# Kernel optimization log

Measured on AMD Instinct MI355X. Metric: run time of the kernel, lower is better.

## Reference

```python
import jax, jax.numpy as jnp
import numpy as np

RES = 7          # pooler_resolution
SR = 2           # sampling_ratio
SCALES = (0.25, 0.125, 0.0625)  # 1/stride for the 3 FPN levels


def _bilinear(feat, ys, xs):
    # feat [C,H,W]; ys, xs [N,S,S] sample coords; returns [C,N,S,S]
    C, H, W = feat.shape
    valid = (ys > -1.0) & (ys < H) & (xs > -1.0) & (xs < W)
    y = jnp.clip(ys, 0.0, H - 1)
    x = jnp.clip(xs, 0.0, W - 1)
    y0 = jnp.floor(y).astype(jnp.int32)
    x0 = jnp.floor(x).astype(jnp.int32)
    y1 = jnp.minimum(y0 + 1, H - 1)
    x1 = jnp.minimum(x0 + 1, W - 1)
    ly = y - y0; lx = x - x0
    hy = 1.0 - ly; hx = 1.0 - lx
    v = (feat[:, y0, x0] * (hy * hx) + feat[:, y0, x1] * (hy * lx)
         + feat[:, y1, x0] * (ly * hx) + feat[:, y1, x1] * (ly * lx))
    return v * valid


def _roi_align(feat, boxes, scale):
    # feat [C,H,W], boxes [N,4] (t,l,b,r) in image coords, aligned=True
    t, l, b, r = (boxes[:, 0], boxes[:, 1], boxes[:, 2], boxes[:, 3])
    sy = t * scale - 0.5
    sx = l * scale - 0.5
    bh = (b - t) * scale / RES
    bw = (r - l) * scale / RES
    S = RES * SR
    g = (jnp.arange(S, dtype=feat.dtype) + 0.5) / SR  # sample offsets in bin units
    ys = sy[:, None] + g[None, :] * bh[:, None]  # [N,S]
    xs = sx[:, None] + g[None, :] * bw[:, None]
    N = boxes.shape[0]
    Y = jnp.broadcast_to(ys[:, :, None], (N, S, S))
    X = jnp.broadcast_to(xs[:, None, :], (N, S, S))
    v = _bilinear(feat, Y, X)                      # [C,N,S,S]
    C = feat.shape[0]
    v = v.reshape(C, N, RES, SR, RES, SR).mean(axis=(3, 5))
    return jnp.transpose(v, (1, 0, 2, 3))          # [N,C,RES,RES]


def _forward(feat0, feat1, feat2, bbox2d, anchor_id,
             fc1_w, fc1_b, bn1_g, bn1_b, fc2_w, fc2_b, bn2_g, bn2_b,
             cate_w, cate_b, bbox3d_w, bbox3d_b, yawc_w, yawc_b,
             yawr_w, yawr_b, hgt_w, hgt_b):
    # yxhw -> tlbr (mu.convert_box_format_yxhw_to_tlbr)
    cy, cx, h, w = (bbox2d[..., 0], bbox2d[..., 1], bbox2d[..., 2], bbox2d[..., 3])
    tlbr = jnp.stack([cy - h / 2, cx - w / 2, cy + h / 2, cx + w / 2], axis=-1)
    level = anchor_id // 3  # [B,N] per-box FPN level (anchor_id // 3 == i routing)
    feats = [feat0, feat1, feat2]
    B, N = level.shape
    C = feat0.shape[1]
    pooled = jnp.zeros((B, N, C, RES, RES), dtype=feat0.dtype)
    for i in range(3):
        al = jax.vmap(lambda fm, bx, s=SCALES[i]: _roi_align(fm, bx, s))(feats[i], tlbr)
        pooled = jnp.where((level == i)[:, :, None, None, None], al, pooled)
    x = pooled.reshape(B * N, -1)  # [B*N, C*RES*RES]
    eps = 1e-5
    for Wt, bb, g2, b2 in ((fc1_w, fc1_b, bn1_g, bn1_b), (fc2_w, fc2_b, bn2_g, bn2_b)):
        x = x @ Wt + bb
        mu = x.mean(0)
        var = x.var(0)
        x = jax.nn.relu((x - mu) / jnp.sqrt(var + eps) * g2 + b2)
    cate = x @ cate_w + cate_b
    bbox3d = x @ bbox3d_w + bbox3d_b
    yawc = x @ yawc_w + yawc_b
    yawr = x @ yawr_w + yawr_b
    hgt = x @ hgt_w + hgt_b
    out = jnp.concatenate([cate, bbox3d, yawc, yawr, hgt], axis=-1)  # [B*N, 100]
    return out.reshape(B, N, -1)


def setup_inputs() -> dict:
    key = jax.random.key(0)
    ks = jax.random.split(key, 24)
    B, N, C = 4, 512, 256
    FC = 1024
    IMG = 512.0
    NUM_CLASSES, BOX_DIM, BINS = 3, 6, 12
    feat0 = jax.random.normal(ks[0], (B, C, 128, 128), jnp.float32)
    feat1 = jax.random.normal(ks[1], (B, C, 64, 64), jnp.float32)
    feat2 = jax.random.normal(ks[2], (B, C, 32, 32), jnp.float32)
    cy = jax.random.uniform(ks[3], (B, N)) * IMG
    cx = jax.random.uniform(ks[4], (B, N)) * IMG
    h = 16.0 + jax.random.uniform(ks[5], (B, N)) * 240.0
    w = 16.0 + jax.random.uniform(ks[6], (B, N)) * 240.0
    bbox2d = jnp.stack([cy, cx, h, w], axis=-1)
    anchor_id = jax.random.randint(ks[7], (B, N), 0, 9, dtype=jnp.int32)
    in_dim = C * RES * RES  # 12544
    fc1_w = jax.random.normal(ks[8], (in_dim, FC), jnp.float32) / np.sqrt(in_dim)
    fc1_b = jnp.zeros((FC,), jnp.float32)
    bn1_g = jnp.ones((FC,), jnp.float32)
    bn1_b = jnp.zeros((FC,), jnp.float32)
    fc2_w = jax.random.normal(ks[9], (FC, FC), jnp.float32) / np.sqrt(FC)
    fc2_b = jnp.zeros((FC,), jnp.float32)
    bn2_g = jnp.ones((FC,), jnp.float32)
    bn2_b = jnp.zeros((FC,), jnp.float32)
    cate_w = jax.random.normal(ks[10], (FC, NUM_CLASSES + 1), jnp.float32) * 0.01
    cate_b = jnp.zeros((NUM_CLASSES + 1,), jnp.float32)
    bbox3d_w = jax.random.normal(ks[11], (FC, NUM_CLASSES * BOX_DIM), jnp.float32) * 0.001
    bbox3d_b = jnp.zeros((NUM_CLASSES * BOX_DIM,), jnp.float32)
    yawc_w = jax.random.normal(ks[12], (FC, NUM_CLASSES * BINS), jnp.float32) * 0.001
    yawc_b = jnp.zeros((NUM_CLASSES * BINS,), jnp.float32)
    yawr_w = jax.random.normal(ks[13], (FC, NUM_CLASSES * BINS), jnp.float32) * 0.001
    yawr_b = jnp.zeros((NUM_CLASSES * BINS,), jnp.float32)
    hgt_w = jax.random.normal(ks[14], (FC, NUM_CLASSES * 2), jnp.float32) * 0.001
    hgt_b = jnp.zeros((NUM_CLASSES * 2,), jnp.float32)
    return {
        'feat0': feat0, 'feat1': feat1, 'feat2': feat2,
        'bbox2d': bbox2d, 'anchor_id': anchor_id,
        'fc1_w': fc1_w, 'fc1_b': fc1_b, 'bn1_g': bn1_g, 'bn1_b': bn1_b,
        'fc2_w': fc2_w, 'fc2_b': fc2_b, 'bn2_g': bn2_g, 'bn2_b': bn2_b,
        'cate_w': cate_w, 'cate_b': cate_b, 'bbox3d_w': bbox3d_w, 'bbox3d_b': bbox3d_b,
        'yawc_w': yawc_w, 'yawc_b': yawc_b, 'yawr_w': yawr_w, 'yawr_b': yawr_b,
        'hgt_w': hgt_w, 'hgt_b': hgt_b,
    }


def reference(feat0, feat1, feat2, bbox2d, anchor_id,
              fc1_w, fc1_b, bn1_g, bn1_b, fc2_w, fc2_b, bn2_g, bn2_b,
              cate_w, cate_b, bbox3d_w, bbox3d_b, yawc_w, yawc_b,
              yawr_w, yawr_b, hgt_w, hgt_b):
    return _forward(feat0, feat1, feat2, bbox2d, anchor_id,
                    fc1_w, fc1_b, bn1_g, bn1_b, fc2_w, fc2_b, bn2_g, bn2_b,
                    cate_w, cate_b, bbox3d_w, bbox3d_b, yawc_w, yawc_b,
                    yawr_w, yawr_b, hgt_w, hgt_b)
```

## Files before the change

kernel.cpp:

```cpp
#include <hip/hip_runtime.h>
#include <hip/hip_bf16.h>

typedef unsigned short u16;
typedef unsigned int u32;
typedef __bf16 bf16x8 __attribute__((ext_vector_type(8)));
typedef float f32x4 __attribute__((ext_vector_type(4)));

#define RESOLUTION 7
#define SR 2
#define SS 14
#define NSAMP 196

static __device__ __forceinline__ u16 f2bf(float f) {
    __hip_bfloat16 t = __float2bfloat16(f);
    return *reinterpret_cast<u16*>(&t);
}
static __device__ __forceinline__ float bf2f(u16 h) {
    return __uint_as_float(((u32)h) << 16);
}

static __device__ __forceinline__ void load_lds16(const u16* g, u16* l) {
    __builtin_amdgcn_global_load_lds(
        (const __attribute__((address_space(1))) unsigned int*)g,
        (__attribute__((address_space(3))) unsigned int*)l, 16, 0, 0);
}

__global__ __launch_bounds__(256) void transpose_feat3_kernel(
    const float* __restrict__ f0, const float* __restrict__ f1,
    const float* __restrict__ f2, u16* __restrict__ tf0,
    u16* __restrict__ tf1, u16* __restrict__ tf2) {
    int b = blockIdx.y;
    int bx = blockIdx.x;
    const float* in;
    u16* out;
    int HW, hw0;
    if (bx < 256)      { in = f0; out = tf0; HW = 16384; hw0 = bx * 64; }
    else if (bx < 320) { in = f1; out = tf1; HW = 4096;  hw0 = (bx - 256) * 64; }
    else               { in = f2; out = tf2; HW = 1024;  hw0 = (bx - 320) * 64; }

    __shared__ u16 tile[256][65];
    int hw4 = (threadIdx.x & 15) * 4;
    int cs = threadIdx.x >> 4;
    for (int cc = 0; cc < 256; cc += 16) {
        int c = cc + cs;
        float4 v = *(const float4*)&in[((size_t)(b * 256 + c)) * HW + hw0 + hw4];
        tile[c][hw4 + 0] = f2bf(v.x);
        tile[c][hw4 + 1] = f2bf(v.y);
        tile[c][hw4 + 2] = f2bf(v.z);
        tile[c][hw4 + 3] = f2bf(v.w);
    }
    __syncthreads();

    int ro = threadIdx.x >> 5;
    int co = (threadIdx.x & 31) * 8;
    for (int i = 0; i < 64; i += 8) {
        int hw = i + ro;
        union { uint4 v; u16 h[8]; } o;
        #pragma unroll
        for (int j = 0; j < 8; ++j) o.h[j] = tile[co + j][hw];
        *(uint4*)&out[((size_t)b * HW + hw0 + hw) * 256 + co] = o.v;
    }
}

__global__ __launch_bounds__(256) void transpose_w2_kernel(
    const float* __restrict__ in1, const float* __restrict__ in2,
    u16* __restrict__ w1t, u16* __restrict__ w2t,
    float4* __restrict__ y4) {
    int bx = blockIdx.x, n0 = blockIdx.y * 64;
    const float* in;
    u16* out;
    int K, kp0, perm;
    if (bx < 196) { in = in1; out = w1t; K = 12544; kp0 = bx * 64; perm = 1; }
    else          { in = in2; out = w2t; K = 1024;  kp0 = (bx - 196) * 64; perm = 0; }

    int fid = (blockIdx.y * 212 + bx) * 256 + threadIdx.x;
    if (fid < 524288) y4[fid] = make_float4(0.f, 0.f, 0.f, 0.f);

    __shared__ u16 tile[64][65];
    int nn4 = (threadIdx.x & 15) * 4;
    int ks = threadIdx.x >> 4;
    for (int i = 0; i < 64; i += 16) {
        int kp = kp0 + ks + i;
        int k = perm ? ((kp & 255) * 49 + (kp >> 8)) : kp;
        float4 v = *(const float4*)&in[(size_t)k * 1024 + n0 + nn4];
        tile[ks + i][nn4 + 0] = f2bf(v.x);
        tile[ks + i][nn4 + 1] = f2bf(v.y);
        tile[ks + i][nn4 + 2] = f2bf(v.z);
        tile[ks + i][nn4 + 3] = f2bf(v.w);
    }
    __syncthreads();

    int nw = threadIdx.x >> 3, ko = (threadIdx.x & 7) * 8;
    for (int i = 0; i < 2; ++i) {
        int n = nw + i * 32;
        union { uint4 v; u16 h[8]; } o;
        #pragma unroll
        for (int j = 0; j < 8; ++j) o.h[j] = tile[ko + j][n];
        *(uint4*)&out[(size_t)(n0 + n) * K + kp0 + ko] = o.v;
    }
}

__global__ void head_prep_kernel(
    const float* __restrict__ cate_w, const float* __restrict__ bbox3d_w,
    const float* __restrict__ yawc_w, const float* __restrict__ yawr_w,
    const float* __restrict__ hgt_w,
    const float* __restrict__ cate_b, const float* __restrict__ bbox3d_b,
    const float* __restrict__ yawc_b, const float* __restrict__ yawr_b,
    const float* __restrict__ hgt_b,
    u16* __restrict__ whT, float* __restrict__ outp) {
    int idx = blockIdx.x * blockDim.x + threadIdx.x;
    if (idx < 128 * 1024) {
        int n = idx >> 10, k = idx & 1023;
        float v = 0.f;
        if (n < 4)        v = cate_w[k * 4 + n];
        else if (n < 22)  v = bbox3d_w[k * 18 + (n - 4)];
        else if (n < 58)  v = yawc_w[k * 36 + (n - 22)];
        else if (n < 94)  v = yawr_w[k * 36 + (n - 58)];
        else if (n < 100) v = hgt_w[k * 6 + (n - 94)];
        whT[idx] = f2bf(v);
    }
    if (idx < 2048 * 100) {
        int c = idx - (idx / 100) * 100;
        float v;
        if (c < 4)        v = cate_b[c];
        else if (c < 22)  v = bbox3d_b[c - 4];
        else if (c < 58)  v = yawc_b[c - 22];
        else if (c < 94)  v = yawr_b[c - 58];
        else              v = hgt_b[c - 94];
        outp[idx] = v;
    }
}

__global__ __launch_bounds__(512) void roi_align_v3_kernel(
    const u16* __restrict__ tf0, const u16* __restrict__ tf1,
    const u16* __restrict__ tf2, const float* __restrict__ bbox2d,
    const int* __restrict__ anchor_id, u16* __restrict__ xb) {
    int bn = blockIdx.x;
    int b = bn >> 9;
    int tid = threadIdx.x;

    __shared__ int s_o00[NSAMP], s_o01[NSAMP], s_o10[NSAMP], s_o11[NSAMP];
    __shared__ float s_w00[NSAMP], s_w01[NSAMP], s_w10[NSAMP], s_w11[NSAMP];

    float cy = bbox2d[bn * 4 + 0], cx = bbox2d[bn * 4 + 1];
    float hh = bbox2d[bn * 4 + 2], ww = bbox2d[bn * 4 + 3];
    int lvl = anchor_id[bn] / 3;
    float scale = (lvl == 0) ? 0.25f : ((lvl == 1) ? 0.125f : 0.0625f);
    int H = (lvl == 0) ? 128 : ((lvl == 1) ? 64 : 32);
    int W = H;

    float t = cy - hh * 0.5f, l = cx - ww * 0.5f;
    float btm = cy + hh * 0.5f, r = cx + ww * 0.5f;
    float sy = t * scale - 0.5f, sx = l * scale - 0.5f;
    float bh = (btm - t) * scale * (1.0f / RESOLUTION);
    float bw = (r - l) * scale * (1.0f / RESOLUTION);

    if (tid < NSAMP) {
        int i = tid / SS, j = tid % SS;
        float gi = (i + 0.5f) * (1.0f / SR);
        float gj = (j + 0.5f) * (1.0f / SR);
        float y = sy + gi * bh, x = sx + gj * bw;
        float valid = (y > -1.0f && y < (float)H && x > -1.0f && x < (float)W)
                          ? 0.25f : 0.0f;
        y = fminf(fmaxf(y, 0.0f), (float)(H - 1));
        x = fminf(fmaxf(x, 0.0f), (float)(W - 1));
        int y0 = (int)floorf(y), x0 = (int)floorf(x);
        int y1 = min(y0 + 1, H - 1), x1 = min(x0 + 1, W - 1);
        float ly = y - (float)y0, lx = x - (float)x0;
        float hy = 1.f - ly, hx = 1.f - lx;
        s_o00[tid] = (y0 * W + x0) * 256;
        s_o01[tid] = (y0 * W + x1) * 256;
        s_o10[tid] = (y1 * W + x0) * 256;
        s_o11[tid] = (y1 * W + x1) * 256;
        s_w00[tid] = hy * hx * valid;
        s_w01[tid] = hy * lx * valid;
        s_w10[tid] = ly * hx * valid;
        s_w11[tid] = ly * lx * valid;
    }
    __syncthreads();

    const u16* fb = (lvl == 0) ? (tf0 + (size_t)b * 16384 * 256)
                  : (lvl == 1) ? (tf1 + (size_t)b * 4096 * 256)
                               : (tf2 + (size_t)b * 1024 * 256);
    int g = tid >> 5;
    int c0 = (tid & 31) * 8;
    u16* xr = xb + (size_t)bn * 12544;

    #pragma unroll
    for (int ii = 0; ii < 4; ++ii) {
        int bin = g + ii * 16;
        if (bin < 49) {
            int ph = bin / 7, pw = bin % 7;
            float a[8] = {0.f, 0.f, 0.f, 0.f, 0.f, 0.f, 0.f, 0.f};
            #pragma unroll
            for (int dy = 0; dy < SR; ++dy) {
                #pragma unroll
                for (int dx = 0; dx < SR; ++dx) {
                    int si = (ph * SR + dy) * SS + (pw * SR + dx);
                    int o00 = s_o00[si], o01 = s_o01[si];
                    int o10 = s_o10[si], o11 = s_o11[si];
                    float w00 = s_w00[si], w01 = s_w01[si];
                    float w10 = s_w10[si], w11 = s_w11[si];
                    union { uint4 v; u16 h[8]; } u0, u1, u2, u3;
                    u0.v = *(const uint4*)(fb + o00 + c0);
                    u1.v = *(const uint4*)(fb + o01 + c0);
                    u2.v = *(const uint4*)(fb + o10 + c0);
                    u3.v = *(const uint4*)(fb + o11 + c0);
                    #pragma unroll
                    for (int j = 0; j < 8; ++j) {
                        a[j] = fmaf(bf2f(u0.h[j]), w00, a[j]);
                        a[j] = fmaf(bf2f(u1.h[j]), w01, a[j]);
                        a[j] = fmaf(bf2f(u2.h[j]), w10, a[j]);
                        a[j] = fmaf(bf2f(u3.h[j]), w11, a[j]);
                    }
                }
            }
            union { uint4 v; u16 h[8]; } o;
            #pragma unroll
            for (int j = 0; j < 8; ++j) o.h[j] = f2bf(a[j]);
            *(uint4*)&xr[bin * 256 + c0] = o.v;
        }
    }
}

__global__ __launch_bounds__(256) void gemm_splitk_kernel(
    const u16* __restrict__ A, const u16* __restrict__ BT,
    float* __restrict__ Y, int ldY, int nmax, int K, int KC) {
    __shared__ u16 la[2][128 * 32];
    __shared__ u16 lb[2][128 * 32];
    int m0 = blockIdx.x * 128;
    int n0 = blockIdx.y * 128;
    int kbeg = blockIdx.z * KC;
    int tid = threadIdx.x;
    int w = tid >> 6, lane = tid & 63;
    int wm = (w >> 1) * 64, wn = (w & 1) * 64;

    int idx1 = tid + 256;
    const u16* gA0 = A + (size_t)(m0 + (tid >> 2)) * K + (tid & 3) * 8 + kbeg;
    const u16* gA1 = A + (size_t)(m0 + (idx1 >> 2)) * K + (idx1 & 3) * 8 + kbeg;
    const u16* gB0 = BT + (size_t)(n0 + (tid >> 2)) * K + (tid & 3) * 8 + kbeg;
    const u16* gB1 = BT + (size_t)(n0 + (idx1 >> 2)) * K + (idx1 & 3) * 8 + kbeg;
    u16* lA0a = la[0] + w * 512;
    u16* lA1a = la[0] + 2048 + w * 512;
    u16* lB0a = lb[0] + w * 512;
    u16* lB1a = lb[0] + 2048 + w * 512;
    u16* lA0b = la[1] + w * 512;
    u16* lA1b = la[1] + 2048 + w * 512;
    u16* lB0b = lb[1] + w * 512;
    u16* lB1b = lb[1] + 2048 + w * 512;

    f32x4 acc[4][4] = {};
    int row16 = lane & 15, q8 = (lane >> 4) * 8;

    for (int k0 = 0; k0 < KC; k0 += 64) {
        load_lds16(gA0 + k0, lA0a);
        load_lds16(gA1 + k0, lA1a);
        load_lds16(gB0 + k0, lB0a);
        load_lds16(gB1 + k0, lB1a);
        load_lds16(gA0 + k0 + 32, lA0b);
        load_lds16(gA1 + k0 + 32, lA1b);
        load_lds16(gB0 + k0 + 32, lB0b);
        load_lds16(gB1 + k0 + 32, lB1b);
        __syncthreads();

        #pragma unroll
        for (int h = 0; h < 2; ++h) {
            bf16x8 af[4], bf[4];
            #pragma unroll
            for (int tm = 0; tm < 4; ++tm)
                af[tm] = *(const bf16x8*)&la[h][(wm + tm * 16 + row16) * 32 + q8];
            #pragma unroll
            for (int tn = 0; tn < 4; ++tn)
                bf[tn] = *(const bf16x8*)&lb[h][(wn + tn * 16 + row16) * 32 + q8];
            #pragma unroll
            for (int tm = 0; tm < 4; ++tm)
                #pragma unroll
                for (int tn = 0; tn < 4; ++tn)
                    acc[tm][tn] = __builtin_amdgcn_mfma_f32_16x16x32_bf16(
                        af[tm], bf[tn], acc[tm][tn], 0, 0, 0);
        }
        __syncthreads();
    }

    int col = lane & 15, qr = lane >> 4;
    #pragma unroll
    for (int tm = 0; tm < 4; ++tm) {
        #pragma unroll
        for (int tn = 0; tn < 4; ++tn) {
            int nn = n0 + wn + tn * 16 + col;
            if (nn < nmax) {
                #pragma unroll
                for (int rg = 0; rg < 4; ++rg) {
                    int mm = m0 + wm + tm * 16 + qr * 4 + rg;
                    unsafeAtomicAdd(&Y[(size_t)mm * ldY + nn], acc[tm][tn][rg]);
                }
            }
        }
    }
}

__global__ __launch_bounds__(256) void bn_stats_part_kernel(
    const float* __restrict__ y, float* __restrict__ part, int N) {
    int c4 = blockIdx.x * 256 + (threadIdx.x & 63) * 4;
    int rg = threadIdx.x >> 6;
    int r0 = blockIdx.y * 32;
    float4 s = make_float4(0.f, 0.f, 0.f, 0.f);
    float4 q = make_float4(0.f, 0.f, 0.f, 0.f);
    for (int i = 0; i < 8; ++i) {
        int r = r0 + rg + i * 4;
        float4 v = *(const float4*)&y[(size_t)r * N + c4];
        s.x += v.x; s.y += v.y; s.z += v.z; s.w += v.w;
        q.x += v.x * v.x; q.y += v.y * v.y; q.z += v.z * v.z; q.w += v.w * v.w;
    }
    __shared__ float4 ls[4][64], lq[4][64];
    ls[rg][threadIdx.x & 63] = s;
    lq[rg][threadIdx.x & 63] = q;
    __syncthreads();
    if (rg == 0) {
        int cx = threadIdx.x & 63;
        #pragma unroll
        for (int g = 1; g < 4; ++g) {
            float4 a = ls[g][cx], b = lq[g][cx];
            s.x += a.x; s.y += a.y; s.z += a.z; s.w += a.w;
            q.x += b.x; q.y += b.y; q.z += b.z; q.w += b.w;
        }
        float* po = part + (size_t)blockIdx.y * 2048;
        *(float4*)&po[c4] = s;
        *(float4*)&po[1024 + c4] = q;
    }
}

__global__ __launch_bounds__(256) void bn_stats_final_kernel(
    const float* __restrict__ part, float* __restrict__ stats, int M, int nchunk) {
    int col = blockIdx.x * 256 + threadIdx.x;
    float s = 0.f, q = 0.f;
    for (int ch = 0; ch < nchunk; ++ch) {
        s += part[(size_t)ch * 2048 + col];
        q += part[(size_t)ch * 2048 + 1024 + col];
    }
    float mean = s / (float)M;
    float var = q / (float)M - mean * mean;
    stats[col] = mean;
    stats[1024 + col] = rsqrtf(var + 1e-5f);
}

__global__ void bn_apply_kernel(float* __restrict__ y,
                                const float* __restrict__ stats,
                                const float* __restrict__ g,
                                const float* __restrict__ b,
                                u16* __restrict__ xo, int total4, int zero_y) {
    int idx = blockIdx.x * blockDim.x + threadIdx.x;
    if (idx >= total4) return;
    int e0 = idx * 4;
    int col = e0 & 1023;
    float4 v = *(const float4*)&y[e0];
    float4 mu = *(const float4*)&stats[col];
    float4 rs = *(const float4*)&stats[1024 + col];
    float4 gg = *(const float4*)&g[col];
    float4 bb = *(const float4*)&b[col];
    ushort4 o;
    o.x = f2bf(fmaxf((v.x - mu.x) * rs.x * gg.x + bb.x, 0.f));
    o.y = f2bf(fmaxf((v.y - mu.y) * rs.y * gg.y + bb.y, 0.f));
    o.z = f2bf(fmaxf((v.z - mu.z) * rs.z * gg.z + bb.z, 0.f));
    o.w = f2bf(fmaxf((v.w - mu.w) * rs.w * gg.w + bb.w, 0.f));
    *(ushort4*)&xo[e0] = o;
    if (zero_y)
        *(float4*)&y[e0] = make_float4(0.f, 0.f, 0.f, 0.f);
}

extern "C" void kernel_launch(void* const* d_in, const int* in_sizes, int n_in,
                              void* d_out, int out_size, void* d_ws, size_t ws_size,
                              hipStream_t stream) {
    const float* feat0   = (const float*)d_in[0];
    const float* feat1   = (const float*)d_in[1];
    const float* feat2   = (const float*)d_in[2];
    const float* bbox2d  = (const float*)d_in[3];
    const int*   anchor  = (const int*)d_in[4];
    const float* fc1_w   = (const float*)d_in[5];
    const float* bn1_g   = (const float*)d_in[7];
    const float* bn1_b   = (const float*)d_in[8];
    const float* fc2_w   = (const float*)d_in[9];
    const float* bn2_g   = (const float*)d_in[11];
    const float* bn2_b   = (const float*)d_in[12];
    const float* cate_w  = (const float*)d_in[13];
    const float* cate_b  = (const float*)d_in[14];
    const float* bbox3d_w= (const float*)d_in[15];
    const float* bbox3d_b= (const float*)d_in[16];
    const float* yawc_w  = (const float*)d_in[17];
    const float* yawc_b  = (const float*)d_in[18];
    const float* yawr_w  = (const float*)d_in[19];
    const float* yawr_b  = (const float*)d_in[20];
    const float* hgt_w   = (const float*)d_in[21];
    const float* hgt_b   = (const float*)d_in[22];

    const int B = 4, N = 512, FC = 1024;
    const int M = B * N;
    const int K1 = 12544;

    char* base = (char*)d_ws;
    u16* xb = (u16*)base;
    char* ub = base + 51380224;
    u16* tf0 = (u16*)ub;
    u16* tf1 = (u16*)(ub + 33554432);
    u16* tf2 = (u16*)(ub + 41943040);
    u16* w1t = (u16*)ub;
    u16* w2t = (u16*)(ub + 25690112);
    float* y   = (float*)(ub + 27787264);
    u16* x1b = (u16*)(ub + 36175872);
    float* part = (float*)(ub + 40370176);
    char* tail = ub + 44040192;
    float* stats = (float*)tail;
    u16*   whT   = (u16*)(tail + 8192);
    float* outp  = (float*)d_out;

    head_prep_kernel<<<(M * 100 + 255) / 256, 256, 0, stream>>>(
        cate_w, bbox3d_w, yawc_w, yawr_w, hgt_w,
        cate_b, bbox3d_b, yawc_b, yawr_b, hgt_b, whT, outp);

    transpose_feat3_kernel<<<dim3(336, B), 256, 0, stream>>>(
        feat0, feat1, feat2, tf0, tf1, tf2);

    roi_align_v3_kernel<<<M, 512, 0, stream>>>(tf0, tf1, tf2, bbox2d, anchor, xb);

    transpose_w2_kernel<<<dim3(212, FC / 64), 256, 0, stream>>>(
        fc1_w, fc2_w, w1t, w2t, (float4*)y);

    gemm_splitk_kernel<<<dim3(M / 128, FC / 128, 4), 256, 0, stream>>>(
        xb, w1t, y, FC, FC, K1, K1 / 4);
    bn_stats_part_kernel<<<dim3(FC / 256, M / 32), 256, 0, stream>>>(y, part, FC);
    bn_stats_final_kernel<<<FC / 256, 256, 0, stream>>>(part, stats, M, M / 32);
    bn_apply_kernel<<<(M * FC / 4 + 255) / 256, 256, 0, stream>>>(
        y, stats, bn1_g, bn1_b, x1b, M * FC / 4, 1);

    gemm_splitk_kernel<<<dim3(M / 128, FC / 128, 4), 256, 0, stream>>>(
        x1b, w2t, y, FC, FC, FC, FC / 4);
    bn_stats_part_kernel<<<dim3(FC / 256, M / 32), 256, 0, stream>>>(y, part, FC);
    bn_stats_final_kernel<<<FC / 256, 256, 0, stream>>>(part, stats, M, M / 32);
    bn_apply_kernel<<<(M * FC / 4 + 255) / 256, 256, 0, stream>>>(
        y, stats, bn2_g, bn2_b, x1b, M * FC / 4, 0);

    gemm_splitk_kernel<<<dim3(M / 128, 1, 16), 256, 0, stream>>>(
        x1b, whT, outp, 100, 100, FC, FC / 16);
}
```

Baseline: 441.1 us.

## Group ROIs by FPN level and swizzle split-K GEMM workgroup order

Adds a single-block sort kernel that buckets ROI indices by pyramid level, so ROI-align blocks launched together read from the same feature map and share cache. It also remaps GEMM workgroup IDs with a stride-8 swizzle, which changes how tiles land across XCDs and L2. The costs are an extra small kernel launch and unordered atomic placement within each level. The swizzle assumes the workgroup count divides by 8, which holds for the current grid.

```diff
diff --git a/kernel.cpp b/kernel.cpp
--- a/kernel.cpp
+++ b/kernel.cpp
@@ -131,11 +131,37 @@
     }
 }
 
+__global__ __launch_bounds__(1024) void roi_sort_kernel(
+    const int* __restrict__ anchor_id, int* __restrict__ list) {
+    __shared__ int cnt[3], base[3];
+    if (threadIdx.x < 3) cnt[threadIdx.x] = 0;
+    __syncthreads();
+    int lv[2];
+    #pragma unroll
+    for (int i = 0; i < 2; ++i) {
+        int r = threadIdx.x * 2 + i;
+        lv[i] = anchor_id[r] / 3;
+        atomicAdd(&cnt[lv[i]], 1);
+    }
+    __syncthreads();
+    if (threadIdx.x == 0) {
+        base[0] = 0; base[1] = cnt[0]; base[2] = cnt[0] + cnt[1];
+    }
+    __syncthreads();
+    #pragma unroll
+    for (int i = 0; i < 2; ++i) {
+        int r = threadIdx.x * 2 + i;
+        int pos = atomicAdd(&base[lv[i]], 1);
+        list[pos] = r;
+    }
+}
+
 __global__ __launch_bounds__(512) void roi_align_v3_kernel(
     const u16* __restrict__ tf0, const u16* __restrict__ tf1,
     const u16* __restrict__ tf2, const float* __restrict__ bbox2d,
-    const int* __restrict__ anchor_id, u16* __restrict__ xb) {
-    int bn = blockIdx.x;
+    const int* __restrict__ anchor_id, const int* __restrict__ list,
+    u16* __restrict__ xb) {
+    int bn = list[blockIdx.x];
     int b = bn >> 9;
     int tid = threadIdx.x;
 
@@ -226,11 +252,19 @@
 __global__ __launch_bounds__(256) void gemm_splitk_kernel(
     const u16* __restrict__ A, const u16* __restrict__ BT,
     float* __restrict__ Y, int ldY, int nmax, int K, int KC) {
+    int nwg = gridDim.x * gridDim.y * gridDim.z;
+    int lin = blockIdx.x + gridDim.x * (blockIdx.y + gridDim.y * blockIdx.z);
+    int swz = (lin & 7) * (nwg >> 3) + (lin >> 3);
+    int bx = swz % gridDim.x;
+    int rem = swz / gridDim.x;
+    int by = rem % gridDim.y;
+    int bz = rem / gridDim.y;
+
     __shared__ u16 la[2][128 * 32];
     __shared__ u16 lb[2][128 * 32];
-    int m0 = blockIdx.x * 128;
-    int n0 = blockIdx.y * 128;
-    int kbeg = blockIdx.z * KC;
+    int m0 = bx * 128;
+    int n0 = by * 128;
+    int kbeg = bz * KC;
     int tid = threadIdx.x;
     int w = tid >> 6, lane = tid & 63;
     int wm = (w >> 1) * 64, wn = (w & 1) * 64;
@@ -411,16 +445,19 @@
     char* tail = ub + 44040192;
     float* stats = (float*)tail;
     u16*   whT   = (u16*)(tail + 8192);
+    int*   rlist = (int*)(tail + 8192 + 262144);
     float* outp  = (float*)d_out;
 
     head_prep_kernel<<<(M * 100 + 255) / 256, 256, 0, stream>>>(
         cate_w, bbox3d_w, yawc_w, yawr_w, hgt_w,
         cate_b, bbox3d_b, yawc_b, yawr_b, hgt_b, whT, outp);
 
+    roi_sort_kernel<<<1, 1024, 0, stream>>>(anchor, rlist);
     transpose_feat3_kernel<<<dim3(336, B), 256, 0, stream>>>(
         feat0, feat1, feat2, tf0, tf1, tf2);
 
-    roi_align_v3_kernel<<<M, 512, 0, stream>>>(tf0, tf1, tf2, bbox2d, anchor, xb);
+    roi_align_v3_kernel<<<M, 512, 0, stream>>>(
+        tf0, tf1, tf2, bbox2d, anchor, rlist, xb);
 
     transpose_w2_kernel<<<dim3(212, FC / 64), 256, 0, stream>>>(
         fc1_w, fc2_w, w1t, w2t, (float4*)y);
```

Result: slower. 459.2 us (+4.1%).

## Deduplicate bilinear taps per ROI bin and swizzle split-K GEMM workgroups

Applied to the files above, without the earlier changes.

The ROI align kernel now builds a compacted list of unique feature offsets and summed weights for each output bin, skipping invalid samples. Taps shared between overlapping samples (common for small boxes) are loaded once instead of several times, and loads are issued in pairs. The setup now runs on only 49 threads, each doing a serial linear search, which lengthens the prologue. Separately, the split-K GEMM remaps its workgroup IDs with an XCD-style swizzle so neighbouring tiles land on the same chiplet for cache reuse.

```diff
diff --git a/kernel.cpp b/kernel.cpp
--- a/kernel.cpp
+++ b/kernel.cpp
@@ -131,7 +131,7 @@
     }
 }
 
-__global__ __launch_bounds__(512) void roi_align_v3_kernel(
+__global__ __launch_bounds__(512) void roi_align_v4_kernel(
     const u16* __restrict__ tf0, const u16* __restrict__ tf1,
     const u16* __restrict__ tf2, const float* __restrict__ bbox2d,
     const int* __restrict__ anchor_id, u16* __restrict__ xb) {
@@ -139,8 +139,9 @@
     int b = bn >> 9;
     int tid = threadIdx.x;
 
-    __shared__ int s_o00[NSAMP], s_o01[NSAMP], s_o10[NSAMP], s_o11[NSAMP];
-    __shared__ float s_w00[NSAMP], s_w01[NSAMP], s_w10[NSAMP], s_w11[NSAMP];
+    __shared__ int s_cnt[49];
+    __shared__ int s_off[49 * 16];
+    __shared__ float s_wt[49 * 16];
 
     float cy = bbox2d[bn * 4 + 0], cx = bbox2d[bn * 4 + 1];
     float hh = bbox2d[bn * 4 + 2], ww = bbox2d[bn * 4 + 3];
@@ -155,27 +156,47 @@
     float bh = (btm - t) * scale * (1.0f / RESOLUTION);
     float bw = (r - l) * scale * (1.0f / RESOLUTION);
 
-    if (tid < NSAMP) {
-        int i = tid / SS, j = tid % SS;
-        float gi = (i + 0.5f) * (1.0f / SR);
-        float gj = (j + 0.5f) * (1.0f / SR);
-        float y = sy + gi * bh, x = sx + gj * bw;
-        float valid = (y > -1.0f && y < (float)H && x > -1.0f && x < (float)W)
-                          ? 0.25f : 0.0f;
-        y = fminf(fmaxf(y, 0.0f), (float)(H - 1));
-        x = fminf(fmaxf(x, 0.0f), (float)(W - 1));
-        int y0 = (int)floorf(y), x0 = (int)floorf(x);
-        int y1 = min(y0 + 1, H - 1), x1 = min(x0 + 1, W - 1);
-        float ly = y - (float)y0, lx = x - (float)x0;
-        float hy = 1.f - ly, hx = 1.f - lx;
-        s_o00[tid] = (y0 * W + x0) * 256;
-        s_o01[tid] = (y0 * W + x1) * 256;
-        s_o10[tid] = (y1 * W + x0) * 256;
-        s_o11[tid] = (y1 * W + x1) * 256;
-        s_w00[tid] = hy * hx * valid;
-        s_w01[tid] = hy * lx * valid;
-        s_w10[tid] = ly * hx * valid;
-        s_w11[tid] = ly * lx * valid;
+    if (tid < 49) {
+        int ph = tid / 7, pw = tid % 7;
+        int base = tid * 16;
+        int n = 0;
+        #pragma unroll
+        for (int dy = 0; dy < SR; ++dy) {
+            #pragma unroll
+            for (int dx = 0; dx < SR; ++dx) {
+                int i = ph * SR + dy, j = pw * SR + dx;
+                float gi = (i + 0.5f) * (1.0f / SR);
+                float gj = (j + 0.5f) * (1.0f / SR);
+                float y = sy + gi * bh, x = sx + gj * bw;
+                bool valid = (y > -1.0f && y < (float)H &&
+                              x > -1.0f && x < (float)W);
+                if (valid) {
+                    y = fminf(fmaxf(y, 0.0f), (float)(H - 1));
+                    x = fminf(fmaxf(x, 0.0f), (float)(W - 1));
+                    int y0 = (int)floorf(y), x0 = (int)floorf(x);
+                    int y1 = min(y0 + 1, H - 1), x1 = min(x0 + 1, W - 1);
+                    float ly = y - (float)y0, lx = x - (float)x0;
+                    float hy = 1.f - ly, hx = 1.f - lx;
+                    int o4[4] = {(y0 * W + x0) * 256, (y0 * W + x1) * 256,
+                                 (y1 * W + x0) * 256, (y1 * W + x1) * 256};
+                    float w4[4] = {hy * hx * 0.25f, hy * lx * 0.25f,
+                                   ly * hx * 0.25f, ly * lx * 0.25f};
+                    #pragma unroll
+                    for (int c = 0; c < 4; ++c) {
+                        int o = o4[c];
+                        float w = w4[c];
+                        int hit = -1;
+                        for (int rr = 0; rr < n; ++rr)
+                            if (s_off[base + rr] == o) { hit = rr; break; }
+                        if (hit >= 0) s_wt[base + hit] += w;
+                        else { s_off[base + n] = o; s_wt[base + n] = w; ++n; }
+                    }
+                }
+            }
+        }
+        if (n == 0) { s_off[base] = 0; s_wt[base] = 0.f; n = 1; }
+        if (n & 1) { s_off[base + n] = s_off[base]; s_wt[base + n] = 0.f; ++n; }
+        s_cnt[tid] = n;
     }
     __syncthreads();
 
@@ -190,29 +211,19 @@
     for (int ii = 0; ii < 4; ++ii) {
         int bin = g + ii * 16;
         if (bin < 49) {
-            int ph = bin / 7, pw = bin % 7;
+            int n = s_cnt[bin];
+            int base = bin * 16;
             float a[8] = {0.f, 0.f, 0.f, 0.f, 0.f, 0.f, 0.f, 0.f};
-            #pragma unroll
-            for (int dy = 0; dy < SR; ++dy) {
+            for (int rr = 0; rr < n; rr += 2) {
+                int o0 = s_off[base + rr], o1 = s_off[base + rr + 1];
+                float w0 = s_wt[base + rr], w1 = s_wt[base + rr + 1];
+                union { uint4 v; u16 h[8]; } u0, u1;
+                u0.v = *(const uint4*)(fb + o0 + c0);
+                u1.v = *(const uint4*)(fb + o1 + c0);
                 #pragma unroll
-                for (int dx = 0; dx < SR; ++dx) {
-                    int si = (ph * SR + dy) * SS + (pw * SR + dx);
-                    int o00 = s_o00[si], o01 = s_o01[si];
-                    int o10 = s_o10[si], o11 = s_o11[si];
-                    float w00 = s_w00[si], w01 = s_w01[si];
-                    float w10 = s_w10[si], w11 = s_w11[si];
-                    union { uint4 v; u16 h[8]; } u0, u1, u2, u3;
-                    u0.v = *(const uint4*)(fb + o00 + c0);
-                    u1.v = *(const uint4*)(fb + o01 + c0);
-                    u2.v = *(const uint4*)(fb + o10 + c0);
-                    u3.v = *(const uint4*)(fb + o11 + c0);
-                    #pragma unroll
-                    for (int j = 0; j < 8; ++j) {
-                        a[j] = fmaf(bf2f(u0.h[j]), w00, a[j]);
-                        a[j] = fmaf(bf2f(u1.h[j]), w01, a[j]);
-                        a[j] = fmaf(bf2f(u2.h[j]), w10, a[j]);
-                        a[j] = fmaf(bf2f(u3.h[j]), w11, a[j]);
-                    }
+                for (int j = 0; j < 8; ++j) {
+                    a[j] = fmaf(bf2f(u0.h[j]), w0, a[j]);
+                    a[j] = fmaf(bf2f(u1.h[j]), w1, a[j]);
                 }
             }
             union { uint4 v; u16 h[8]; } o;
@@ -226,11 +237,19 @@
 __global__ __launch_bounds__(256) void gemm_splitk_kernel(
     const u16* __restrict__ A, const u16* __restrict__ BT,
     float* __restrict__ Y, int ldY, int nmax, int K, int KC) {
+    int nwg = gridDim.x * gridDim.y * gridDim.z;
+    int lin = blockIdx.x + gridDim.x * (blockIdx.y + gridDim.y * blockIdx.z);
+    int swz = (lin & 7) * (nwg >> 3) + (lin >> 3);
+    int bx = swz % gridDim.x;
+    int rem = swz / gridDim.x;
+    int by = rem % gridDim.y;
+    int bz = rem / gridDim.y;
+
     __shared__ u16 la[2][128 * 32];
     __shared__ u16 lb[2][128 * 32];
-    int m0 = blockIdx.x * 128;
-    int n0 = blockIdx.y * 128;
-    int kbeg = blockIdx.z * KC;
+    int m0 = bx * 128;
+    int n0 = by * 128;
+    int kbeg = bz * KC;
     int tid = threadIdx.x;
     int w = tid >> 6, lane = tid & 63;
     int wm = (w >> 1) * 64, wn = (w & 1) * 64;
@@ -420,7 +439,8 @@
     transpose_feat3_kernel<<<dim3(336, B), 256, 0, stream>>>(
         feat0, feat1, feat2, tf0, tf1, tf2);
 
-    roi_align_v3_kernel<<<M, 512, 0, stream>>>(tf0, tf1, tf2, bbox2d, anchor, xb);
+    roi_align_v4_kernel<<<M, 512, 0, stream>>>(
+        tf0, tf1, tf2, bbox2d, anchor, xb);
 
     transpose_w2_kernel<<<dim3(212, FC / 64), 256, 0, stream>>>(
         fc1_w, fc2_w, w1t, w2t, (float4*)y);
```

New measurement: 459.5 us. +4.2%, slower.
